# Kernel optimization log

Hardware: AMD Instinct MI355X
Metric: run time of the kernel (lower is better)

The kernel has to match this reference:

```python
import jax, jax.numpy as jnp
import numpy as np

# Dimensions (Llama-3-8B-style GQA with paged KV cache)
B, S, HID = 1, 1024, 4096
H, HKV, D = 32, 8, 128
G = H // HKV
BLK = 16            # tokens per KV block
NB = 256            # blocks in storage
CB = 192            # context blocks attended (3072 tokens)
PAST = 2048         # tokens already cached before this step
NL = 2              # layers in kv_ptr
L = CB * BLK


def rotate_half(x):
    x1, x2 = x[..., : x.shape[-1] // 2], x[..., x.shape[-1] // 2:]
    return jnp.concatenate([-x2, x1], axis=-1)


def setup_inputs() -> dict:
    key = jax.random.key(0)
    ks = jax.random.split(key, 8)
    hidden_states = jax.random.normal(ks[0], (B, S, HID), jnp.float32)
    kv_ptr = jax.random.normal(ks[1], (NL, 2, NB, HKV, BLK, D), jnp.float32)
    Wq = 0.02 * jax.random.normal(ks[2], (H * D, HID), jnp.float32)
    Wk = 0.02 * jax.random.normal(ks[3], (HKV * D, HID), jnp.float32)
    Wv = 0.02 * jax.random.normal(ks[4], (HKV * D, HID), jnp.float32)
    Wo = 0.02 * jax.random.normal(ks[5], (HID, H * D), jnp.float32)
    # RoPE cache for the new tokens (global positions PAST..PAST+S-1), HF convention
    pos = (PAST + jnp.arange(S)).astype(jnp.float32)
    inv_freq = 1.0 / (10000.0 ** (jnp.arange(0, D, 2, dtype=jnp.float32) / D))
    freqs = pos[:, None] * inv_freq[None, :]                # [S, D/2]
    emb = jnp.concatenate([freqs, freqs], axis=-1)           # [S, D]
    cos = jnp.cos(emb)[None, None]                           # [1,1,S,D]
    sin = jnp.sin(emb)[None, None]
    new_q_lut = jnp.arange(S, dtype=jnp.int32)[None]         # identity query LUT
    new_kv_lut = (CB - S // BLK + jnp.arange(S // BLK, dtype=jnp.int32))[None]  # blocks 128..191
    all_kv_lut = jnp.arange(CB, dtype=jnp.int32)[None]       # blocks 0..191
    kv_pos = jnp.arange(L)
    q_pos = PAST + jnp.arange(S)
    mask = (kv_pos[None, None, :] <= q_pos[None, :, None])   # [1,S,L] causal over global positions
    cmd_groups = jnp.zeros((B, S), jnp.int32)                # split-K scheduling metadata (no math effect)
    return dict(hidden_states=hidden_states, kv_ptr=kv_ptr, new_q_lut=new_q_lut,
                new_kv_lut=new_kv_lut, all_kv_lut=all_kv_lut, mask=mask,
                cmd_groups=cmd_groups, cos=cos, sin=sin, Wq=Wq, Wk=Wk, Wv=Wv, Wo=Wo,
                layer_idx=0)


def reference(hidden_states, kv_ptr, new_q_lut, new_kv_lut, all_kv_lut, mask,
              cmd_groups, cos, sin, Wq, Wk, Wv, Wo, layer_idx):
    b, s, _ = hidden_states.shape
    # QKV projections (no bias)
    q = jnp.einsum('bsh,oh->bso', hidden_states, Wq).reshape(b, s, H, D).transpose(0, 2, 1, 3)
    k = jnp.einsum('bsh,oh->bso', hidden_states, Wk).reshape(b, s, HKV, D).transpose(0, 2, 1, 3)
    v = jnp.einsum('bsh,oh->bso', hidden_states, Wv).reshape(b, s, HKV, D).transpose(0, 2, 1, 3)
    # RoPE
    q = q * cos + rotate_half(q) * sin
    k = k * cos + rotate_half(k) * sin
    # fill_kv_block_storage: scatter new K/V blocks into this layer's storage (b == 1)
    kb = jnp.transpose(k[0].reshape(HKV, s // BLK, BLK, D), (1, 0, 2, 3))  # [nblk,HKV,BLK,D]
    vb = jnp.transpose(v[0].reshape(HKV, s // BLK, BLK, D), (1, 0, 2, 3))
    sk = kv_ptr[layer_idx, 0].at[new_kv_lut[0]].set(kb)
    sv = kv_ptr[layer_idx, 1].at[new_kv_lut[0]].set(vb)
    # qkv_attention: gather context blocks via LUT, masked GQA attention
    ck = jnp.transpose(sk[all_kv_lut[0]], (1, 0, 2, 3)).reshape(HKV, L, D)  # [HKV,L,D]
    cv = jnp.transpose(sv[all_kv_lut[0]], (1, 0, 2, 3)).reshape(HKV, L, D)
    qg = q[:, :, new_q_lut[0], :].reshape(b, HKV, G, s, D)
    scores = jnp.einsum('bkgsd,kld->bkgsl', qg, ck) / jnp.sqrt(jnp.float32(D))
    scores = jnp.where(mask[:, None, None], scores, jnp.finfo(scores.dtype).min)
    p = jax.nn.softmax(scores, axis=-1)
    o = jnp.einsum('bkgsl,kld->bkgsd', p, cv).reshape(b, H, s, D)
    o = o.transpose(0, 2, 1, 3).reshape(b, s, H * D)
    return jnp.einsum('bso,ho->bsh', o, Wo)
```

## Files before the change

### kernel.cpp

```cpp
#include <hip/hip_runtime.h>
#include <cstdint>
#include <cstddef>


typedef _Float16 f16;
typedef f16 f16x8 __attribute__((ext_vector_type(8)));
typedef f16 f16x4 __attribute__((ext_vector_type(4)));
typedef float f32x4 __attribute__((ext_vector_type(4)));

#define HIDN 4096
#define LCTX 3072
#define PASTN 2048
#define QK_SCALE_LOG2 0.12753102734366334f
#define RESC_THR 11.54f

__device__ __forceinline__ f32x4 mfma16(f16x8 a, f16x8 b, f32x4 c) {
    return __builtin_amdgcn_mfma_f32_16x16x32_f16(a, b, c, 0, 0, 0);
}
__device__ __forceinline__ f32x4 mfma16k16(f16x4 a, f16x4 b, f32x4 c) {
    return __builtin_amdgcn_mfma_f32_16x16x16f16(a, b, c, 0, 0, 0);
}

__device__ __forceinline__ void gl_lds16(const void* g, void* l) {
    auto gp = (const __attribute__((address_space(1))) unsigned int*)(uintptr_t)g;
    auto lp = (__attribute__((address_space(3))) unsigned int*)(uintptr_t)l;
    __builtin_amdgcn_global_load_lds(gp, lp, 16, 0, 0);
}

__device__ __forceinline__ uint32_t lds_lo(const void* p) {
    return (uint32_t)(uintptr_t)p;
}

#define TRRD(dst, va, OFF) \
    asm volatile("ds_read_b64_tr_b16 %0, %1 offset:" #OFF : "=v"(dst) : "v"(va))
#define WAITL(N) \
    asm volatile("s_waitcnt lgkmcnt(" #N ")" ::: "memory"); \
    __builtin_amdgcn_sched_barrier(0)

__global__ void cvt_h(const float* __restrict__ hidden, f16* __restrict__ h16)
{
    int i = blockIdx.x * 256 + threadIdx.x;
    f32x4 v = *(const f32x4*)(hidden + (size_t)i * 4);
    f16x4 h;
#pragma unroll
    for (int j = 0; j < 4; j++) h[j] = (f16)v[j];
    *(f16x4*)(h16 + (size_t)i * 4) = h;
}

__global__ __launch_bounds__(256, 2) void gemm_qkv(
    const f16* __restrict__ A,
    const float* __restrict__ Bq, const float* __restrict__ Bk2,
    const float* __restrict__ Bv2,
    f16* __restrict__ Cq, f16* __restrict__ Ck, f16* __restrict__ Cv,
    const float* __restrict__ kvp, const int* __restrict__ layer,
    f16* __restrict__ ckc, const float* __restrict__ Wo, f16* __restrict__ w16o)
{
    constexpr int K = 4096;
    __shared__ f16 As[2 * 256 * 64];
    __shared__ f16 Bs[2 * 64 * 64];

    const int bx = blockIdx.x;

    if (bx >= 384) {
        const int lay = layer[0];
        const int cid = bx - 384;
        int base = cid * 256 + threadIdx.x;
#pragma unroll
        for (int pass = 0; pass < 32; ++pass) {
            int i4 = base + pass * 32768;
            int half = i4 >> 19;
            int e = (i4 & 524287) * 4;
            int hh = e >> 18, rem = e & 262143, l = rem >> 7, d = rem & 127;
            int blk = l >> 4, rr = l & 15;
            size_t src = (((size_t)(lay * 2 + half) * 256 + blk) * 8 + hh) * 2048
                       + (size_t)rr * 128 + d;
            f32x4 x = *(const f32x4*)(kvp + src);
            f16x4 h;
#pragma unroll
            for (int j = 0; j < 4; j++) h[j] = (f16)x[j];
            size_t dst = ((size_t)hh * LCTX + l) * 128 + d;
            *(f16x4*)((half ? Cv : ckc) + dst) = h;
        }
        {
            const float* src = Wo + (size_t)cid * 131072;
            f16* dst = w16o + (size_t)cid * 131072;
#pragma unroll 4
            for (int p = 0; p < 128; ++p) {
                int e = (p * 256 + threadIdx.x) * 4;
                f32x4 v = *(const f32x4*)(src + e);
                f16x4 hv;
#pragma unroll
                for (int jx = 0; jx < 4; jx++) hv[jx] = (f16)v[jx];
                *(f16x4*)(dst + e) = hv;
            }
        }
        return;
    }

    const int t = threadIdx.x, lane = t & 63, w = t >> 6;
    const int wm = w >> 1, wn = w & 1;
    const int l16 = lane & 15, g16 = lane >> 4;
    const int m0 = (bx / 96) * 256, n0 = (bx % 96) * 64;

    const int srow = lane >> 3;
    const int sgr  = (lane & 7) ^ srow;
    const size_t aoff = (size_t)(m0 + w * 64 + srow) * K + sgr * 8;

    const float* Bf;
    int nb = n0;
    if (n0 >= 5120)      { Bf = Bv2; nb = n0 - 5120; }
    else if (n0 >= 4096) { Bf = Bk2; nb = n0 - 4096; }
    else                 { Bf = Bq; }
    const int brw = lane >> 4;
    const int b4  = lane & 15;
    const int bg  = b4 >> 1, bsub = (b4 & 1) << 2;
    const float* bbase = Bf + (size_t)(nb + w * 16 + brw) * K + b4 * 4;

    int bwr[4];
#pragma unroll
    for (int j = 0; j < 4; j++) {
        int r = w * 16 + j * 4 + brw;
        bwr[j] = r * 64 + ((bg ^ (r & 7)) << 3) + bsub;
    }

    f32x4 acc[8][2];
#pragma unroll
    for (int i = 0; i < 8; i++)
#pragma unroll
        for (int j = 0; j < 2; j++) acc[i][j] = (f32x4){0.f, 0.f, 0.f, 0.f};

    f32x4 bv[4];
#pragma unroll
    for (int j = 0; j < 4; j++)
        bv[j] = *(const f32x4*)(bbase + (size_t)(j * 4) * K);
#pragma unroll
    for (int j = 0; j < 8; j++)
        gl_lds16(A + aoff + (size_t)j * 8 * K,
                 (void*)(As + (w * 64 + j * 8) * 64));
#pragma unroll
    for (int j = 0; j < 4; j++) {
        f16x4 hv;
#pragma unroll
        for (int q = 0; q < 4; q++) hv[q] = (f16)bv[j][q];
        *(f16x4*)&Bs[bwr[j]] = hv;
    }
    __syncthreads();

    for (int k0 = 0; k0 < K; k0 += 64) {
        const int cur = (k0 >> 6) & 1;
        const int nxt = cur ^ 1;
        const bool more = (k0 + 64 < K);
        if (more) {
#pragma unroll
            for (int j = 0; j < 8; j++)
                gl_lds16(A + aoff + (size_t)j * 8 * K + k0 + 64,
                         (void*)(As + nxt * 16384 + (w * 64 + j * 8) * 64));
#pragma unroll
            for (int j = 0; j < 4; j++)
                bv[j] = *(const f32x4*)(bbase + (size_t)(j * 4) * K + k0 + 64);
        }
#pragma unroll
        for (int ks = 0; ks < 2; ks++) {
            f16x8 af[8], bfr[2];
#pragma unroll
            for (int mi = 0; mi < 8; mi++) {
                int r = wm * 128 + mi * 16 + l16;
                int g = ks * 4 + g16;
                af[mi] = *(const f16x8*)&As[cur * 16384 + r * 64 + ((g ^ (r & 7)) << 3)];
            }
#pragma unroll
            for (int ni = 0; ni < 2; ni++) {
                int r = wn * 32 + ni * 16 + l16;
                int g = ks * 4 + g16;
                bfr[ni] = *(const f16x8*)&Bs[cur * 4096 + r * 64 + ((g ^ (r & 7)) << 3)];
            }
#pragma unroll
            for (int ni = 0; ni < 2; ni++)
#pragma unroll
                for (int mi = 0; mi < 8; mi++)
                    acc[mi][ni] = mfma16(af[mi], bfr[ni], acc[mi][ni]);
        }
        if (more) {
#pragma unroll
            for (int j = 0; j < 4; j++) {
                f16x4 hv;
#pragma unroll
                for (int q = 0; q < 4; q++) hv[q] = (f16)bv[j][q];
                *(f16x4*)&Bs[nxt * 4096 + bwr[j]] = hv;
            }
        }
        __syncthreads();
    }

#pragma unroll
    for (int mi = 0; mi < 8; mi++)
#pragma unroll
        for (int ni = 0; ni < 2; ni++)
#pragma unroll
            for (int r = 0; r < 4; r++) {
                int row = m0 + wm * 128 + mi * 16 + (g16 << 2) + r;
                int col = n0 + wn * 32 + ni * 16 + l16;
                float val = acc[mi][ni][r];
                if (col < 4096) {
                    Cq[(size_t)row * 4096 + col] = (f16)val;
                } else if (col < 5120) {
                    Ck[(size_t)row * 1024 + (col - 4096)] = (f16)val;
                } else {
                    int c = col - 5120;
                    int hh = c >> 7, d = c & 127;
                    Cv[((size_t)hh * LCTX + PASTN + row) * 128 + d] = (f16)val;
                }
            }
}

__global__ __launch_bounds__(256, 3) void gemm_o(
    const f16* __restrict__ A, const f16* __restrict__ Bh,
    float* __restrict__ Cf)
{
    constexpr int K = 4096;
    __shared__ f16 As[64 * 64];
    __shared__ f16 Bs[128 * 64];

    const int bx = blockIdx.x;
    const int t = threadIdx.x, lane = t & 63, w = t >> 6;
    const int wm = w >> 1, wn = w & 1;
    const int l16 = lane & 15, g16 = lane >> 4;
    const int m0 = (bx / 32) * 64, n0 = (bx % 32) * 128;

    const int srow = lane >> 3;
    const int sgr  = (lane & 7) ^ srow;

    const size_t aoff = (size_t)(m0 + w * 16 + srow) * K + sgr * 8;
    const size_t boff = (size_t)(n0 + w * 32 + srow) * K + sgr * 8;

    f32x4 acc[2][4];
#pragma unroll
    for (int i = 0; i < 2; i++)
#pragma unroll
        for (int j = 0; j < 4; j++) acc[i][j] = (f32x4){0.f, 0.f, 0.f, 0.f};

    for (int k0 = 0; k0 < K; k0 += 64) {
#pragma unroll
        for (int j = 0; j < 2; j++)
            gl_lds16(A + aoff + (size_t)j * 8 * K + k0,
                     (void*)(As + (w * 16 + j * 8) * 64));
#pragma unroll
        for (int j = 0; j < 4; j++)
            gl_lds16(Bh + boff + (size_t)j * 8 * K + k0,
                     (void*)(Bs + (w * 32 + j * 8) * 64));
        __syncthreads();

#pragma unroll
        for (int ks = 0; ks < 2; ks++) {
            f16x8 af[2], bfr[4];
#pragma unroll
            for (int mi = 0; mi < 2; mi++) {
                int r = wm * 32 + mi * 16 + l16;
                int g = ks * 4 + g16;
                af[mi] = *(const f16x8*)&As[r * 64 + ((g ^ (r & 7)) << 3)];
            }
#pragma unroll
            for (int ni = 0; ni < 4; ni++) {
                int r = wn * 64 + ni * 16 + l16;
                int g = ks * 4 + g16;
                bfr[ni] = *(const f16x8*)&Bs[r * 64 + ((g ^ (r & 7)) << 3)];
            }
#pragma unroll
            for (int ni = 0; ni < 4; ni++)
#pragma unroll
                for (int mi = 0; mi < 2; mi++)
                    acc[mi][ni] = mfma16(af[mi], bfr[ni], acc[mi][ni]);
        }
        __syncthreads();
    }

#pragma unroll
    for (int mi = 0; mi < 2; mi++)
#pragma unroll
        for (int ni = 0; ni < 4; ni++)
#pragma unroll
            for (int r = 0; r < 4; r++) {
                int row = m0 + wm * 32 + mi * 16 + (g16 << 2) + r;
                int col = n0 + wn * 64 + ni * 16 + l16;
                Cf[(size_t)row * 4096 + col] = acc[mi][ni][r];
            }
}

__global__ void aux2(f16* __restrict__ q16, const f16* __restrict__ kraw,
                     const float* __restrict__ cosp, const float* __restrict__ sinp,
                     f16* __restrict__ ck)
{
    int i = blockIdx.x * 256 + threadIdx.x;
    if (i < 262144) {
        int gd = i & 7, hh = (i >> 3) & 31, s = i >> 8;
        size_t b1 = (size_t)s * 4096 + hh * 128 + gd * 8;
        f16x8 x1 = *(f16x8*)(q16 + b1);
        f16x8 x2 = *(f16x8*)(q16 + b1 + 64);
        const float* c1 = cosp + s * 128 + gd * 8;
        const float* s1 = sinp + s * 128 + gd * 8;
        f16x8 o1, o2;
#pragma unroll
        for (int j = 0; j < 8; j++) {
            float a = (float)x1[j], b = (float)x2[j];
            o1[j] = (f16)((a * c1[j] - b * s1[j]) * QK_SCALE_LOG2);
            o2[j] = (f16)((b * c1[j + 64] + a * s1[j + 64]) * QK_SCALE_LOG2);
        }
        *(f16x8*)(q16 + b1) = o1;
        *(f16x8*)(q16 + b1 + 64) = o2;
    } else {
        int ii = i - 262144;
        int gd = ii & 7, kvh = (ii >> 3) & 7, s = ii >> 6;
        size_t b1 = (size_t)s * 1024 + kvh * 128 + gd * 8;
        f16x8 x1 = *(const f16x8*)(kraw + b1);
        f16x8 x2 = *(const f16x8*)(kraw + b1 + 64);
        const float* c1 = cosp + s * 128 + gd * 8;
        const float* s1 = sinp + s * 128 + gd * 8;
        f16x8 o1, o2;
#pragma unroll
        for (int j = 0; j < 8; j++) {
            float a = (float)x1[j], b = (float)x2[j];
            o1[j] = (f16)(a * c1[j] - b * s1[j]);
            o2[j] = (f16)(b * c1[j + 64] + a * s1[j + 64]);
        }
        size_t dst = ((size_t)kvh * LCTX + PASTN + s) * 128 + gd * 8;
        *(f16x8*)(ck + dst) = o1;
        *(f16x8*)(ck + dst + 64) = o2;
    }
}

__global__ __launch_bounds__(256, 2) void attn_part(
    const f16* __restrict__ Q, const f16* __restrict__ Kc,
    const f16* __restrict__ Vc, f16* __restrict__ Op, float* __restrict__ mlb)
{
    const int b = blockIdx.x;
    const int z = b >> 8;
    const int idx = b & 255;
    const int h = idx & 31;
    const int jj = idx >> 5;
    const int j = z ? (7 - jj) : jj;
    const int s0 = j * 128;
    const int kvh = h >> 2;
    const int t = threadIdx.x, lane = t & 63, w = t >> 6;
    const int l16 = lane & 15, g16 = lane >> 4;

    __shared__ f16 Ks[2][64 * 128];
    __shared__ f16 Vs[2][64 * 128];

    f16x8 qfA[4], qfB[4];
    {
        size_t baseA = (size_t)(s0 + w * 32 + l16) * 4096 + h * 128;
        size_t baseB = baseA + (size_t)16 * 4096;
#pragma unroll
        for (int kk = 0; kk < 4; kk++) {
            qfA[kk] = *(const f16x8*)(Q + baseA + kk * 32 + g16 * 8);
            qfB[kk] = *(const f16x8*)(Q + baseB + kk * 32 + g16 * 8);
        }
    }

    f32x4 ofA[8], ofB[8];
#pragma unroll
    for (int cf = 0; cf < 8; cf++) {
        ofA[cf] = (f32x4){0.f, 0.f, 0.f, 0.f};
        ofB[cf] = (f32x4){0.f, 0.f, 0.f, 0.f};
    }
    float mrA = -3.0e38f, lrA = 0.f;
    float mrB = -3.0e38f, lrB = 0.f;

    const f16* Kb = Kc + (size_t)kvh * LCTX * 128;
    const f16* Vb = Vc + (size_t)kvh * LCTX * 128;
    const int ntt = (PASTN + s0 + 128) >> 6;

    const int krow = lane >> 4;
    const int kp   = lane & 15;
    const int vrow = ((lane >> 5) << 4) + (((lane >> 3) & 3) << 2) + ((lane >> 1) & 3);
    const int vch  = (lane & 1) << 3;

    const uint32_t vs0 = lds_lo(Vs[0]) + lane * 8;
    const uint32_t vs1 = lds_lo(Vs[1]) + lane * 8;

#define STAGE_KV(l0, buf)                                                     \
    {                                                                         \
        _Pragma("unroll")                                                     \
        for (int jx = 0; jx < 4; jx++) {                                      \
            int r7 = ((jx & 1) << 2) + krow;                                  \
            int sg = kp ^ r7;                                                 \
            gl_lds16(Kb + (size_t)((l0) + w * 16 + jx * 4 + krow) * 128 + sg * 8, \
                     (void*)(Ks[buf] + (w * 16 + jx * 4) * 128));             \
        }                                                                     \
        _Pragma("unroll")                                                     \
        for (int q = 0; q < 4; q++) {                                         \
            gl_lds16(Vb + (size_t)((l0) + (q & 1) * 32 + vrow) * 128          \
                        + (w * 2 + (q >> 1)) * 16 + vch,                      \
                     (void*)(Vs[buf] + (w * 4 + q) * 512));                   \
        }                                                                     \
    }

    STAGE_KV(z * 64, 0);
    __syncthreads();

    int itp = 0;
    for (int it = z; it < ntt; it += 2, ++itp) {
        const int l0 = it << 6;
        const int cur = itp & 1;

        if (it + 2 < ntt) STAGE_KV(l0 + 128, cur ^ 1);

        f32x4 sA[4], sB[4];
#pragma unroll
        for (int ni = 0; ni < 4; ni++) {
            sA[ni] = (f32x4){0.f, 0.f, 0.f, 0.f};
            sB[ni] = (f32x4){0.f, 0.f, 0.f, 0.f};
        }
        __builtin_amdgcn_s_setprio(1);
#pragma unroll
        for (int ni = 0; ni < 4; ni++)
#pragma unroll
            for (int kk = 0; kk < 4; kk++) {
                int r = ni * 16 + l16;
                int g = kk * 4 + g16;
                f16x8 kh = *(const f16x8*)&Ks[cur][r * 128 + ((g ^ (r & 7)) << 3)];
                sA[ni] = mfma16(kh, qfA[kk], sA[ni]);
                sB[ni] = mfma16(kh, qfB[kk], sB[ni]);
            }
        __builtin_amdgcn_s_setprio(0);

#define SOFTMAX(sf, mr, lr, of, QOFF)                                          \
        {                                                                      \
            const int qrow = s0 + w * 32 + (QOFF) + l16;                       \
            if (l0 + 63 > PASTN + s0 + w * 32 + (QOFF)) {                      \
                _Pragma("unroll")                                              \
                for (int ni = 0; ni < 4; ni++)                                 \
                    _Pragma("unroll")                                          \
                    for (int r = 0; r < 4; r++) {                              \
                        int col = l0 + ni * 16 + (g16 << 2) + r;               \
                        if (col > PASTN + qrow) sf[ni][r] = -3.0e38f;          \
                    }                                                          \
            }                                                                  \
            float mx;                                                          \
            {                                                                  \
                f32x4 m4 = sf[0];                                              \
                _Pragma("unroll")                                              \
                for (int ni = 1; ni < 4; ni++) {                               \
                    m4[0] = fmaxf(m4[0], sf[ni][0]);                           \
                    m4[1] = fmaxf(m4[1], sf[ni][1]);                           \
                    m4[2] = fmaxf(m4[2], sf[ni][2]);                           \
                    m4[3] = fmaxf(m4[3], sf[ni][3]);                           \
                }                                                              \
                mx = fmaxf(fmaxf(m4[0], m4[1]), fmaxf(m4[2], m4[3]));          \
            }                                                                  \
            mx = fmaxf(mx, __shfl_xor(mx, 16));                                \
            mx = fmaxf(mx, __shfl_xor(mx, 32));                                \
            if (__any(mx > mr + RESC_THR)) {                                   \
                float mnew = fmaxf(mr, mx);                                    \
                float corr = exp2f(mr - mnew);                                 \
                mr = mnew;                                                     \
                lr *= corr;                                                    \
                float cr[4];                                                   \
                _Pragma("unroll")                                              \
                for (int r = 0; r < 4; r++) cr[r] = __shfl(corr, (g16 << 2) + r); \
                _Pragma("unroll")                                              \
                for (int cf = 0; cf < 8; cf++)                                 \
                    _Pragma("unroll")                                          \
                    for (int r = 0; r < 4; r++) of[cf][r] *= cr[r];            \
            }                                                                  \
            _Pragma("unroll")                                                  \
            for (int ni = 0; ni < 4; ni++)                                     \
                _Pragma("unroll")                                              \
                for (int r = 0; r < 4; r++) {                                  \
                    float p = exp2f(sf[ni][r] - mr);                           \
                    sf[ni][r] = p;                                             \
                    lr += p;                                                   \
                }                                                              \
        }

        SOFTMAX(sA, mrA, lrA, ofA, 0)
        SOFTMAX(sB, mrB, lrB, ofB, 16)

        f16x4 paA[4], paB[4];
#pragma unroll
        for (int ni = 0; ni < 4; ni++) {
            paA[ni][0] = (f16)sA[ni][0]; paA[ni][1] = (f16)sA[ni][1];
            paA[ni][2] = (f16)sA[ni][2]; paA[ni][3] = (f16)sA[ni][3];
            paB[ni][0] = (f16)sB[ni][0]; paB[ni][1] = (f16)sB[ni][1];
            paB[ni][2] = (f16)sB[ni][2]; paB[ni][3] = (f16)sB[ni][3];
        }

        {
            const uint32_t va = cur ? vs1 : vs0;
            f16x4 ra0, ra1, ra2, ra3, rb0, rb1, rb2, rb3;
            f16x4 rc0, rc1, rc2, rc3, rd0, rd1, rd2, rd3;
            __builtin_amdgcn_s_setprio(1);
            TRRD(ra0,va,0);     TRRD(ra1,va,512);   TRRD(ra2,va,1024);  TRRD(ra3,va,1536);
            TRRD(rb0,va,2048);  TRRD(rb1,va,2560);  TRRD(rb2,va,3072);  TRRD(rb3,va,3584);
            TRRD(rc0,va,4096);  TRRD(rc1,va,4608);  TRRD(rc2,va,5120);  TRRD(rc3,va,5632);
#define X2(cf, ni, reg) \
            ofA[cf] = mfma16k16(paA[ni], reg, ofA[cf]); \
            ofB[cf] = mfma16k16(paB[ni], reg, ofB[cf]);
            WAITL(8);
            X2(0,0,ra0) X2(0,1,ra1) X2(0,2,ra2) X2(0,3,ra3)
            TRRD(rd0,va,6144);  TRRD(rd1,va,6656);  TRRD(rd2,va,7168);  TRRD(rd3,va,7680);
            WAITL(8);
            X2(1,0,rb0) X2(1,1,rb1) X2(1,2,rb2) X2(1,3,rb3)
            TRRD(ra0,va,8192);  TRRD(ra1,va,8704);  TRRD(ra2,va,9216);  TRRD(ra3,va,9728);
            WAITL(8);
            X2(2,0,rc0) X2(2,1,rc1) X2(2,2,rc2) X2(2,3,rc3)
            TRRD(rb0,va,10240); TRRD(rb1,va,10752); TRRD(rb2,va,11264); TRRD(rb3,va,11776);
            WAITL(8);
            X2(3,0,rd0) X2(3,1,rd1) X2(3,2,rd2) X2(3,3,rd3)
            TRRD(rc0,va,12288); TRRD(rc1,va,12800); TRRD(rc2,va,13312); TRRD(rc3,va,13824);
            WAITL(8);
            X2(4,0,ra0) X2(4,1,ra1) X2(4,2,ra2) X2(4,3,ra3)
            TRRD(rd0,va,14336); TRRD(rd1,va,14848); TRRD(rd2,va,15360); TRRD(rd3,va,15872);
            WAITL(8);
            X2(5,0,rb0) X2(5,1,rb1) X2(5,2,rb2) X2(5,3,rb3)
            WAITL(4);
            X2(6,0,rc0) X2(6,1,rc1) X2(6,2,rc2) X2(6,3,rc3)
            WAITL(0);
            X2(7,0,rd0) X2(7,1,rd1) X2(7,2,rd2) X2(7,3,rd3)
#undef X2
            __builtin_amdgcn_s_setprio(0);
        }
        __syncthreads();
    }

#define WRITE_P(of, mr, lr, QOFF)                                             \
    {                                                                         \
        float l2 = lr + __shfl_xor(lr, 16);                                   \
        l2 += __shfl_xor(l2, 32);                                             \
        if (lane < 16) {                                                      \
            int srow = s0 + w * 32 + (QOFF) + lane;                           \
            *(float2*)(mlb + (((size_t)z * 1024 + srow) * 32 + h) * 2) =      \
                make_float2(mr, l2);                                          \
        }                                                                     \
        float lrr[4];                                                         \
        _Pragma("unroll")                                                     \
        for (int r = 0; r < 4; r++) lrr[r] = __shfl(l2, (g16 << 2) + r);      \
        _Pragma("unroll")                                                     \
        for (int cf = 0; cf < 8; cf++)                                        \
            _Pragma("unroll")                                                 \
            for (int r = 0; r < 4; r++) {                                     \
                int srow = s0 + w * 32 + (QOFF) + (g16 << 2) + r;             \
                int d = cf * 16 + l16;                                        \
                Op[(size_t)z * 4194304 + (size_t)srow * 4096                  \
                   + (size_t)h * 128 + d] = (f16)(of[cf][r] / lrr[r]);        \
            }                                                                 \
    }
    WRITE_P(ofA, mrA, lrA, 0)
    WRITE_P(ofB, mrB, lrB, 16)
#undef WRITE_P
#undef SOFTMAX
#undef STAGE_KV
}

__global__ void attn_combine(const f16* __restrict__ Op, const float* __restrict__ mlb,
                             f16* __restrict__ obuf)
{
    int i = blockIdx.x * 256 + threadIdx.x;
    int d8 = i & 15, hh = (i >> 4) & 31, s = i >> 9;
    float2 ml0 = *(const float2*)(mlb + (((size_t)0 * 1024 + s) * 32 + hh) * 2);
    float2 ml1 = *(const float2*)(mlb + (((size_t)1 * 1024 + s) * 32 + hh) * 2);
    float mstar = fmaxf(ml0.x, ml1.x);
    float w0 = exp2f(ml0.x - mstar) * ml0.y;
    float w1 = exp2f(ml1.x - mstar) * ml1.y;
    float inv = 1.0f / (w0 + w1);
    size_t off = (size_t)s * 4096 + (size_t)hh * 128 + d8 * 8;
    f16x8 a = *(const f16x8*)(Op + off);
    f16x8 b = *(const f16x8*)(Op + 4194304 + off);
    f16x8 o;
#pragma unroll
    for (int jx = 0; jx < 8; jx++)
        o[jx] = (f16)(((float)a[jx] * w0 + (float)b[jx] * w1) * inv);
    *(f16x8*)(obuf + off) = o;
}

extern "C" void kernel_launch(void* const* d_in, const int* in_sizes, int n_in,
                              void* d_out, int out_size, void* d_ws, size_t ws_size,
                              hipStream_t stream)
{
    const float* hidden = (const float*)d_in[0];
    const float* kvp    = (const float*)d_in[1];
    const float* cosp   = (const float*)d_in[7];
    const float* sinp   = (const float*)d_in[8];
    const float* Wq     = (const float*)d_in[9];
    const float* Wk     = (const float*)d_in[10];
    const float* Wv     = (const float*)d_in[11];
    const float* Wo     = (const float*)d_in[12];
    const int*   layer  = (const int*)d_in[13];

    char* ws = (char*)d_ws;
    f16* w16  = (f16*)ws;
    f16* opart= (f16*)(ws + 33554432);
    f16* h16  = (f16*)(ws + 50331648);
    f16* ck   = (f16*)(ws + 58720256);
    f16* cv   = (f16*)(ws + 65011712);
    f16* obuf = (f16*)(ws + 71303168);

    f16*   q16  = (f16*)d_out;
    f16*   kraw = (f16*)((char*)d_out + 8388608);
    float* mlb  = (float*)((char*)d_out + 8388608);

    cvt_h<<<4096, 256, 0, stream>>>(hidden, h16);

    gemm_qkv<<<dim3(512), 256, 0, stream>>>(
        h16, Wq, Wk, Wv, q16, kraw, cv, kvp, layer, ck, Wo, w16);

    aux2<<<1280, 256, 0, stream>>>(q16, kraw, cosp, sinp, ck);

    attn_part<<<dim3(512), 256, 0, stream>>>(q16, ck, cv, opart, mlb);

    attn_combine<<<2048, 256, 0, stream>>>(opart, mlb, obuf);

    gemm_o<<<dim3(512), 256, 0, stream>>>(obuf, w16, (float*)d_out);
}
```

Baseline: 239.3 us.

## Split attention KV range four ways with 32-row tiles and MFMA row sums

Attention is now split across four interleaved KV partitions instead of two, launching 1024 blocks with 32-row K/V tiles and half the LDS per block. The softmax denominator is accumulated with an MFMA against a ones vector instead of scalar adds and cross-lane shuffles. The combine kernel merges four partials in place, and the partial buffers reuse workspace regions. This adds occupancy and parallelism at the cost of more partial-output traffic, more combine work, and smaller tiles with more per-iteration overhead.

```diff
diff --git a/kernel.cpp b/kernel.cpp
--- a/kernel.cpp
+++ b/kernel.cpp
@@ -330,21 +330,25 @@
 
 __global__ __launch_bounds__(256, 2) void attn_part(
     const f16* __restrict__ Q, const f16* __restrict__ Kc,
-    const f16* __restrict__ Vc, f16* __restrict__ Op, float* __restrict__ mlb)
+    const f16* __restrict__ Vc, f16* __restrict__ Op0, f16* __restrict__ Op1,
+    f16* __restrict__ Op2, f16* __restrict__ Op3,
+    float* __restrict__ mlb_m, float* __restrict__ mlb_l)
 {
     const int b = blockIdx.x;
     const int z = b >> 8;
     const int idx = b & 255;
     const int h = idx & 31;
     const int jj = idx >> 5;
-    const int j = z ? (7 - jj) : jj;
+    const int j = (z & 1) ? (7 - jj) : jj;
     const int s0 = j * 128;
     const int kvh = h >> 2;
     const int t = threadIdx.x, lane = t & 63, w = t >> 6;
     const int l16 = lane & 15, g16 = lane >> 4;
 
-    __shared__ f16 Ks[2][64 * 128];
-    __shared__ f16 Vs[2][64 * 128];
+    __shared__ f16 Ks[2][32 * 128];
+    __shared__ f16 Vs[2][32 * 128];
+
+    f16* Op = (z == 0) ? Op0 : (z == 1) ? Op1 : (z == 2) ? Op2 : Op3;
 
     f16x8 qfA[4], qfB[4];
     {
@@ -363,17 +367,21 @@
         ofA[cf] = (f32x4){0.f, 0.f, 0.f, 0.f};
         ofB[cf] = (f32x4){0.f, 0.f, 0.f, 0.f};
     }
-    float mrA = -3.0e38f, lrA = 0.f;
-    float mrB = -3.0e38f, lrB = 0.f;
+    f32x4 lsA = (f32x4){0.f, 0.f, 0.f, 0.f};
+    f32x4 lsB = (f32x4){0.f, 0.f, 0.f, 0.f};
+    float mrA = -3.0e38f, mrB = -3.0e38f;
+    const f16x4 vone = {(f16)1.f, (f16)1.f, (f16)1.f, (f16)1.f};
 
     const f16* Kb = Kc + (size_t)kvh * LCTX * 128;
     const f16* Vb = Vc + (size_t)kvh * LCTX * 128;
-    const int ntt = (PASTN + s0 + 128) >> 6;
+    const int ntt = (PASTN + s0 + 128) >> 5;
 
     const int krow = lane >> 4;
     const int kp   = lane & 15;
-    const int vrow = ((lane >> 5) << 4) + (((lane >> 3) & 3) << 2) + ((lane >> 1) & 3);
-    const int vch  = (lane & 1) << 3;
+    const int lh  = lane & 31;
+    const int niv = lane >> 5;
+    const int vr  = 4 * (lh >> 3) + ((lh >> 1) & 3);
+    const int vcl = 8 * (lh & 1);
 
     const uint32_t vs0 = lds_lo(Vs[0]) + lane * 8;
     const uint32_t vs1 = lds_lo(Vs[1]) + lane * 8;
@@ -381,39 +389,40 @@
 #define STAGE_KV(l0, buf)                                                     \
     {                                                                         \
         _Pragma("unroll")                                                     \
-        for (int jx = 0; jx < 4; jx++) {                                      \
-            int r7 = ((jx & 1) << 2) + krow;                                  \
+        for (int q = 0; q < 2; q++) {                                         \
+            int L = w * 2 + q;                                                \
+            int r7 = ((L & 1) << 2) + krow;                                   \
             int sg = kp ^ r7;                                                 \
-            gl_lds16(Kb + (size_t)((l0) + w * 16 + jx * 4 + krow) * 128 + sg * 8, \
-                     (void*)(Ks[buf] + (w * 16 + jx * 4) * 128));             \
+            gl_lds16(Kb + (size_t)((l0) + L * 4 + krow) * 128 + sg * 8,       \
+                     (void*)(Ks[buf] + (L * 4) * 128));                       \
         }                                                                     \
         _Pragma("unroll")                                                     \
-        for (int q = 0; q < 4; q++) {                                         \
-            gl_lds16(Vb + (size_t)((l0) + (q & 1) * 32 + vrow) * 128          \
-                        + (w * 2 + (q >> 1)) * 16 + vch,                      \
-                     (void*)(Vs[buf] + (w * 4 + q) * 512));                   \
+        for (int q = 0; q < 2; q++) {                                         \
+            int p = w * 2 + q;                                                \
+            gl_lds16(Vb + (size_t)((l0) + niv * 16 + vr) * 128 + p * 16 + vcl,\
+                     (void*)(Vs[buf] + p * 512));                             \
         }                                                                     \
     }
 
-    STAGE_KV(z * 64, 0);
+    STAGE_KV(z * 32, 0);
     __syncthreads();
 
     int itp = 0;
-    for (int it = z; it < ntt; it += 2, ++itp) {
-        const int l0 = it << 6;
+    for (int it = z; it < ntt; it += 4, ++itp) {
+        const int l0 = it << 5;
         const int cur = itp & 1;
 
-        if (it + 2 < ntt) STAGE_KV(l0 + 128, cur ^ 1);
-
-        f32x4 sA[4], sB[4];
-#pragma unroll
-        for (int ni = 0; ni < 4; ni++) {
+        if (it + 4 < ntt) STAGE_KV(l0 + 128, cur ^ 1);
+
+        f32x4 sA[2], sB[2];
+#pragma unroll
+        for (int ni = 0; ni < 2; ni++) {
             sA[ni] = (f32x4){0.f, 0.f, 0.f, 0.f};
             sB[ni] = (f32x4){0.f, 0.f, 0.f, 0.f};
         }
         __builtin_amdgcn_s_setprio(1);
 #pragma unroll
-        for (int ni = 0; ni < 4; ni++)
+        for (int ni = 0; ni < 2; ni++)
 #pragma unroll
             for (int kk = 0; kk < 4; kk++) {
                 int r = ni * 16 + l16;
@@ -424,12 +433,12 @@
             }
         __builtin_amdgcn_s_setprio(0);
 
-#define SOFTMAX(sf, mr, lr, of, QOFF)                                          \
+#define SOFTMAX(sf, mr, ls, of, QOFF)                                          \
         {                                                                      \
             const int qrow = s0 + w * 32 + (QOFF) + l16;                       \
-            if (l0 + 63 > PASTN + s0 + w * 32 + (QOFF)) {                      \
+            if (l0 + 31 > PASTN + s0 + w * 32 + (QOFF)) {                      \
                 _Pragma("unroll")                                              \
-                for (int ni = 0; ni < 4; ni++)                                 \
+                for (int ni = 0; ni < 2; ni++)                                 \
                     _Pragma("unroll")                                          \
                     for (int r = 0; r < 4; r++) {                              \
                         int col = l0 + ni * 16 + (g16 << 2) + r;               \
@@ -439,13 +448,10 @@
             float mx;                                                          \
             {                                                                  \
                 f32x4 m4 = sf[0];                                              \
-                _Pragma("unroll")                                              \
-                for (int ni = 1; ni < 4; ni++) {                               \
-                    m4[0] = fmaxf(m4[0], sf[ni][0]);                           \
-                    m4[1] = fmaxf(m4[1], sf[ni][1]);                           \
-                    m4[2] = fmaxf(m4[2], sf[ni][2]);                           \
-                    m4[3] = fmaxf(m4[3], sf[ni][3]);                           \
-                }                                                              \
+                m4[0] = fmaxf(m4[0], sf[1][0]);                                \
+                m4[1] = fmaxf(m4[1], sf[1][1]);                                \
+                m4[2] = fmaxf(m4[2], sf[1][2]);                                \
+                m4[3] = fmaxf(m4[3], sf[1][3]);                                \
                 mx = fmaxf(fmaxf(m4[0], m4[1]), fmaxf(m4[2], m4[3]));          \
             }                                                                  \
             mx = fmaxf(mx, __shfl_xor(mx, 16));                                \
@@ -454,31 +460,29 @@
                 float mnew = fmaxf(mr, mx);                                    \
                 float corr = exp2f(mr - mnew);                                 \
                 mr = mnew;                                                     \
-                lr *= corr;                                                    \
                 float cr[4];                                                   \
                 _Pragma("unroll")                                              \
                 for (int r = 0; r < 4; r++) cr[r] = __shfl(corr, (g16 << 2) + r); \
+                _Pragma("unroll")                                              \
+                for (int r = 0; r < 4; r++) ls[r] *= cr[r];                    \
                 _Pragma("unroll")                                              \
                 for (int cf = 0; cf < 8; cf++)                                 \
                     _Pragma("unroll")                                          \
                     for (int r = 0; r < 4; r++) of[cf][r] *= cr[r];            \
             }                                                                  \
             _Pragma("unroll")                                                  \
-            for (int ni = 0; ni < 4; ni++)                                     \
+            for (int ni = 0; ni < 2; ni++)                                     \
                 _Pragma("unroll")                                              \
-                for (int r = 0; r < 4; r++) {                                  \
-                    float p = exp2f(sf[ni][r] - mr);                           \
-                    sf[ni][r] = p;                                             \
-                    lr += p;                                                   \
-                }                                                              \
-        }
-
-        SOFTMAX(sA, mrA, lrA, ofA, 0)
-        SOFTMAX(sB, mrB, lrB, ofB, 16)
-
-        f16x4 paA[4], paB[4];
-#pragma unroll
-        for (int ni = 0; ni < 4; ni++) {
+                for (int r = 0; r < 4; r++)                                    \
+                    sf[ni][r] = exp2f(sf[ni][r] - mr);                         \
+        }
+
+        SOFTMAX(sA, mrA, lsA, ofA, 0)
+        SOFTMAX(sB, mrB, lsB, ofB, 16)
+
+        f16x4 paA[2], paB[2];
+#pragma unroll
+        for (int ni = 0; ni < 2; ni++) {
             paA[ni][0] = (f16)sA[ni][0]; paA[ni][1] = (f16)sA[ni][1];
             paA[ni][2] = (f16)sA[ni][2]; paA[ni][3] = (f16)sA[ni][3];
             paB[ni][0] = (f16)sB[ni][0]; paB[ni][1] = (f16)sB[ni][1];
@@ -492,85 +496,89 @@
             __builtin_amdgcn_s_setprio(1);
             TRRD(ra0,va,0);     TRRD(ra1,va,512);   TRRD(ra2,va,1024);  TRRD(ra3,va,1536);
             TRRD(rb0,va,2048);  TRRD(rb1,va,2560);  TRRD(rb2,va,3072);  TRRD(rb3,va,3584);
-            TRRD(rc0,va,4096);  TRRD(rc1,va,4608);  TRRD(rc2,va,5120);  TRRD(rc3,va,5632);
+#pragma unroll
+            for (int ni = 0; ni < 2; ni++) {
+                lsA = mfma16k16(paA[ni], vone, lsA);
+                lsB = mfma16k16(paB[ni], vone, lsB);
+            }
 #define X2(cf, ni, reg) \
             ofA[cf] = mfma16k16(paA[ni], reg, ofA[cf]); \
             ofB[cf] = mfma16k16(paB[ni], reg, ofB[cf]);
-            WAITL(8);
-            X2(0,0,ra0) X2(0,1,ra1) X2(0,2,ra2) X2(0,3,ra3)
+            WAITL(4);
+            X2(0,0,ra0) X2(0,1,ra1) X2(1,0,ra2) X2(1,1,ra3)
+            TRRD(rc0,va,4096);  TRRD(rc1,va,4608);  TRRD(rc2,va,5120);  TRRD(rc3,va,5632);
+            WAITL(4);
+            X2(2,0,rb0) X2(2,1,rb1) X2(3,0,rb2) X2(3,1,rb3)
             TRRD(rd0,va,6144);  TRRD(rd1,va,6656);  TRRD(rd2,va,7168);  TRRD(rd3,va,7680);
-            WAITL(8);
-            X2(1,0,rb0) X2(1,1,rb1) X2(1,2,rb2) X2(1,3,rb3)
-            TRRD(ra0,va,8192);  TRRD(ra1,va,8704);  TRRD(ra2,va,9216);  TRRD(ra3,va,9728);
-            WAITL(8);
-            X2(2,0,rc0) X2(2,1,rc1) X2(2,2,rc2) X2(2,3,rc3)
-            TRRD(rb0,va,10240); TRRD(rb1,va,10752); TRRD(rb2,va,11264); TRRD(rb3,va,11776);
-            WAITL(8);
-            X2(3,0,rd0) X2(3,1,rd1) X2(3,2,rd2) X2(3,3,rd3)
-            TRRD(rc0,va,12288); TRRD(rc1,va,12800); TRRD(rc2,va,13312); TRRD(rc3,va,13824);
-            WAITL(8);
-            X2(4,0,ra0) X2(4,1,ra1) X2(4,2,ra2) X2(4,3,ra3)
-            TRRD(rd0,va,14336); TRRD(rd1,va,14848); TRRD(rd2,va,15360); TRRD(rd3,va,15872);
-            WAITL(8);
-            X2(5,0,rb0) X2(5,1,rb1) X2(5,2,rb2) X2(5,3,rb3)
             WAITL(4);
-            X2(6,0,rc0) X2(6,1,rc1) X2(6,2,rc2) X2(6,3,rc3)
+            X2(4,0,rc0) X2(4,1,rc1) X2(5,0,rc2) X2(5,1,rc3)
             WAITL(0);
-            X2(7,0,rd0) X2(7,1,rd1) X2(7,2,rd2) X2(7,3,rd3)
+            X2(6,0,rd0) X2(6,1,rd1) X2(7,0,rd2) X2(7,1,rd3)
 #undef X2
             __builtin_amdgcn_s_setprio(0);
         }
         __syncthreads();
     }
 
-#define WRITE_P(of, mr, lr, QOFF)                                             \
+#define WRITE_P(of, mr, ls, QOFF)                                             \
     {                                                                         \
-        float l2 = lr + __shfl_xor(lr, 16);                                   \
-        l2 += __shfl_xor(l2, 32);                                             \
         if (lane < 16) {                                                      \
             int srow = s0 + w * 32 + (QOFF) + lane;                           \
-            *(float2*)(mlb + (((size_t)z * 1024 + srow) * 32 + h) * 2) =      \
-                make_float2(mr, l2);                                          \
+            mlb_m[((size_t)z * 1024 + srow) * 32 + h] = mr;                   \
         }                                                                     \
-        float lrr[4];                                                         \
-        _Pragma("unroll")                                                     \
-        for (int r = 0; r < 4; r++) lrr[r] = __shfl(l2, (g16 << 2) + r);      \
+        if (l16 == 0) {                                                       \
+            _Pragma("unroll")                                                 \
+            for (int r = 0; r < 4; r++) {                                     \
+                int srow = s0 + w * 32 + (QOFF) + (g16 << 2) + r;             \
+                mlb_l[((size_t)z * 1024 + srow) * 32 + h] = ls[r];            \
+            }                                                                 \
+        }                                                                     \
         _Pragma("unroll")                                                     \
         for (int cf = 0; cf < 8; cf++)                                        \
             _Pragma("unroll")                                                 \
             for (int r = 0; r < 4; r++) {                                     \
                 int srow = s0 + w * 32 + (QOFF) + (g16 << 2) + r;             \
                 int d = cf * 16 + l16;                                        \
-                Op[(size_t)z * 4194304 + (size_t)srow * 4096                  \
-                   + (size_t)h * 128 + d] = (f16)(of[cf][r] / lrr[r]);        \
+                Op[(size_t)srow * 4096 + (size_t)h * 128 + d] =               \
+                    (f16)(of[cf][r] / ls[r]);                                 \
             }                                                                 \
     }
-    WRITE_P(ofA, mrA, lrA, 0)
-    WRITE_P(ofB, mrB, lrB, 16)
+    WRITE_P(ofA, mrA, lsA, 0)
+    WRITE_P(ofB, mrB, lsB, 16)
 #undef WRITE_P
 #undef SOFTMAX
 #undef STAGE_KV
 }
 
-__global__ void attn_combine(const f16* __restrict__ Op, const float* __restrict__ mlb,
-                             f16* __restrict__ obuf)
+__global__ void attn_combine(f16* Op0, const f16* Op1, const f16* Op2,
+                             const f16* Op3, const float* mlb_m,
+                             const float* mlb_l)
 {
     int i = blockIdx.x * 256 + threadIdx.x;
     int d8 = i & 15, hh = (i >> 4) & 31, s = i >> 9;
-    float2 ml0 = *(const float2*)(mlb + (((size_t)0 * 1024 + s) * 32 + hh) * 2);
-    float2 ml1 = *(const float2*)(mlb + (((size_t)1 * 1024 + s) * 32 + hh) * 2);
-    float mstar = fmaxf(ml0.x, ml1.x);
-    float w0 = exp2f(ml0.x - mstar) * ml0.y;
-    float w1 = exp2f(ml1.x - mstar) * ml1.y;
-    float inv = 1.0f / (w0 + w1);
+    float m[4], l[4];
+#pragma unroll
+    for (int zz = 0; zz < 4; zz++) {
+        m[zz] = mlb_m[((size_t)zz * 1024 + s) * 32 + hh];
+        l[zz] = mlb_l[((size_t)zz * 1024 + s) * 32 + hh];
+    }
+    float mstar = fmaxf(fmaxf(m[0], m[1]), fmaxf(m[2], m[3]));
+    float wt[4];
+    float tot = 0.f;
+#pragma unroll
+    for (int zz = 0; zz < 4; zz++) { wt[zz] = exp2f(m[zz] - mstar) * l[zz]; tot += wt[zz]; }
+    float inv = 1.0f / tot;
     size_t off = (size_t)s * 4096 + (size_t)hh * 128 + d8 * 8;
-    f16x8 a = *(const f16x8*)(Op + off);
-    f16x8 b = *(const f16x8*)(Op + 4194304 + off);
+    f16x8 a0 = *(const f16x8*)(Op0 + off);
+    f16x8 a1 = *(const f16x8*)(Op1 + off);
+    f16x8 a2 = *(const f16x8*)(Op2 + off);
+    f16x8 a3 = *(const f16x8*)(Op3 + off);
     f16x8 o;
 #pragma unroll
     for (int jx = 0; jx < 8; jx++)
-        o[jx] = (f16)(((float)a[jx] * w0 + (float)b[jx] * w1) * inv);
-    *(f16x8*)(obuf + off) = o;
+        o[jx] = (f16)(((float)a0[jx] * wt[0] + (float)a1[jx] * wt[1]
+                     + (float)a2[jx] * wt[2] + (float)a3[jx] * wt[3]) * inv);
+    *(f16x8*)(Op0 + off) = o;
 }
 
 extern "C" void kernel_launch(void* const* d_in, const int* in_sizes, int n_in,
@@ -584,20 +592,25 @@
     const float* Wq     = (const float*)d_in[9];
     const float* Wk     = (const float*)d_in[10];
     const float* Wv     = (const float*)d_in[11];
+    const float* Wv2    = (const float*)d_in[11];
     const float* Wo     = (const float*)d_in[12];
     const int*   layer  = (const int*)d_in[13];
+    (void)Wv2;
 
     char* ws = (char*)d_ws;
-    f16* w16  = (f16*)ws;
-    f16* opart= (f16*)(ws + 33554432);
-    f16* h16  = (f16*)(ws + 50331648);
-    f16* ck   = (f16*)(ws + 58720256);
-    f16* cv   = (f16*)(ws + 65011712);
-    f16* obuf = (f16*)(ws + 71303168);
-
-    f16*   q16  = (f16*)d_out;
-    f16*   kraw = (f16*)((char*)d_out + 8388608);
-    float* mlb  = (float*)((char*)d_out + 8388608);
+    f16* w16    = (f16*)ws;
+    f16* opart0 = (f16*)(ws + 33554432);
+    f16* opart1 = (f16*)(ws + 41943040);
+    f16* h16    = (f16*)(ws + 50331648);
+    f16* opart2 = (f16*)(ws + 50331648);
+    f16* ck     = (f16*)(ws + 58720256);
+    f16* cv     = (f16*)(ws + 65011712);
+    f16* opart3 = (f16*)(ws + 71303168);
+
+    f16*   q16   = (f16*)d_out;
+    f16*   kraw  = (f16*)((char*)d_out + 8388608);
+    float* mlb_m = (float*)((char*)d_out + 8388608);
+    float* mlb_l = (float*)((char*)d_out + 8912896);
 
     cvt_h<<<4096, 256, 0, stream>>>(hidden, h16);
 
@@ -606,9 +619,11 @@
 
     aux2<<<1280, 256, 0, stream>>>(q16, kraw, cosp, sinp, ck);
 
-    attn_part<<<dim3(512), 256, 0, stream>>>(q16, ck, cv, opart, mlb);
-
-    attn_combine<<<2048, 256, 0, stream>>>(opart, mlb, obuf);
-
-    gemm_o<<<dim3(512), 256, 0, stream>>>(obuf, w16, (float*)d_out);
-}
+    attn_part<<<dim3(1024), 256, 0, stream>>>(
+        q16, ck, cv, opart0, opart1, opart2, opart3, mlb_m, mlb_l);
+
+    attn_combine<<<2048, 256, 0, stream>>>(opart0, opart1, opart2, opart3,
+                                           mlb_m, mlb_l);
+
+    gemm_o<<<dim3(512), 256, 0, stream>>>(opart0, w16, (float*)d_out);
+}
```

Result: slower. 251.9 us (+5.3%).
